# Kernel optimization log

Hardware: AMD Instinct MI355X
Metric: run time of the kernel (lower is better)

The kernel has to match this reference:

```python
import jax, jax.numpy as jnp
import numpy as np

D_MODEL = 1024
N_HEADS = 16
D_K = D_MODEL // N_HEADS
MAX_SEQ = 2048
THETA = 10000.0


def _make_cos_sin():
    # cos_sin[i, k, 0] = cos(i / theta**(2k/d_k)), [.., 1] = sin(...)
    pos = np.arange(MAX_SEQ, dtype=np.float32)[:, None]
    k = np.arange(D_K // 2, dtype=np.float32)[None, :]
    ang = pos / (THETA ** (2.0 * k / D_K))
    return jnp.asarray(np.stack([np.cos(ang), np.sin(ang)], axis=-1), dtype=jnp.float32)


def setup_inputs() -> dict:
    key = jax.random.key(0)
    ks = jax.random.split(key, 5)
    std = 2.0 / (D_MODEL + D_MODEL)
    def w(k):
        return std * jax.random.truncated_normal(k, -3.0, 3.0, (D_MODEL, D_MODEL), dtype=jnp.float32)
    return {
        "x": jax.random.normal(ks[0], (4, 2048, D_MODEL), dtype=jnp.float32),
        "Wq": w(ks[1]),
        "Wk": w(ks[2]),
        "Wv": w(ks[3]),
        "Wo": w(ks[4]),
        "cos_sin": _make_cos_sin(),
        "token_positions": jnp.arange(2048, dtype=jnp.int32),
    }


def _rope(x, cos_sin, pos):
    # x: [B, H, S, d_k]; rotate consecutive pairs
    B, H, S, d = x.shape
    xt = x.reshape(B, H, S, d // 2, 2)
    cos = cos_sin[pos, :, 0]  # [S, d/2]
    sin = cos_sin[pos, :, 1]
    x0, x1 = xt[..., 0], xt[..., 1]
    r0 = cos * x0 - sin * x1
    r1 = sin * x0 + cos * x1
    return jnp.stack([r0, r1], axis=-1).reshape(B, H, S, d)


def reference(x, Wq, Wk, Wv, Wo, cos_sin, token_positions):
    B, S, D = x.shape
    H, d = N_HEADS, D_K
    def proj(W):
        y = jnp.einsum('bsi,oi->bso', x, W)
        return y.reshape(B, S, H, d).transpose(0, 2, 1, 3)  # [B,H,S,d]
    q = _rope(proj(Wq), cos_sin, token_positions)
    k = _rope(proj(Wk), cos_sin, token_positions)
    v = proj(Wv)
    scores = jnp.einsum('bhqd,bhkd->bhqk', q, k) / jnp.sqrt(jnp.float32(d))
    causal = jnp.tril(jnp.ones((S, S), dtype=bool))
    scores = jnp.where(causal, scores, -jnp.inf)
    attn = jax.nn.softmax(scores, axis=-1)
    out = jnp.einsum('bhqk,bhkd->bhqd', attn, v)
    out = out.transpose(0, 2, 1, 3).reshape(B, S, D)
    return jnp.einsum('bsi,oi->bso', out, Wo)
```

## Files before the change

### kernel.cpp

```cpp
#include <hip/hip_runtime.h>

constexpr int B_  = 4;
constexpr int S_  = 2048;
constexpr int D_  = 1024;
constexpr int H_  = 16;
constexpr int DK_ = 64;
constexpr int M_  = B_ * S_;

typedef __attribute__((ext_vector_type(8))) short short8;
typedef __attribute__((ext_vector_type(4))) float f32x4;
typedef __attribute__((ext_vector_type(4))) unsigned short us4;

__device__ __forceinline__ unsigned short f2b(float f) {
  unsigned int u = __float_as_uint(f);
  u += 0x7FFFu + ((u >> 16) & 1u);
  return (unsigned short)(u >> 16);
}
__device__ __forceinline__ float b2f(unsigned short h) {
  return __uint_as_float(((unsigned int)h) << 16);
}
__device__ __forceinline__ unsigned int cvtpk(float lo, float hi) {
  unsigned int w;
  asm("v_cvt_pk_bf16_f32 %0, %1, %2" : "=v"(w) : "v"(lo), "v"(hi));
  return w;
}
__device__ __forceinline__ float exp2v(float x) {
  float r;
  asm("v_exp_f32 %0, %1" : "=v"(r) : "v"(x));
  return r;
}

#define GLOAD16(g, l) __builtin_amdgcn_global_load_lds( \
    (const __attribute__((address_space(1))) unsigned int*)(g), \
    (__attribute__((address_space(3))) unsigned int*)(l), 16, 0, 0)

__global__ __launch_bounds__(256) void conv_kernel(
    const float* __restrict__ x,
    const float* __restrict__ wq, const float* __restrict__ wk, const float* __restrict__ wv,
    unsigned short* __restrict__ xb, unsigned short* __restrict__ wb)
{
  const int NX4 = (M_ * D_) / 4;
  const int NW4 = (3 * D_ * D_) / 4;
  int stride = gridDim.x * blockDim.x;
  for (int i = blockIdx.x * blockDim.x + threadIdx.x; i < NX4 + NW4; i += stride) {
    const float4* src; unsigned short* dst; int o;
    if (i < NX4) { src = (const float4*)x; dst = xb; o = i; }
    else {
      int wi = i - NX4;
      int mat = wi >> 18;
      o = wi & 262143;
      src = (const float4*)(mat == 0 ? wq : (mat == 1 ? wk : wv));
      dst = wb + mat * (D_ * D_);
    }
    float4 v = src[o];
    us4 r; r.x = f2b(v.x); r.y = f2b(v.y); r.z = f2b(v.z); r.w = f2b(v.w);
    *(us4*)(dst + o * 4) = r;
  }
}

__global__ __launch_bounds__(256) void conv_wo_kernel(
    const float* __restrict__ wo, unsigned short* __restrict__ wob)
{
  int i = blockIdx.x * 256 + threadIdx.x;
  float4 v = ((const float4*)wo)[i];
  us4 r; r.x = f2b(v.x); r.y = f2b(v.y); r.z = f2b(v.z); r.w = f2b(v.w);
  *(us4*)(wob + i * 4) = r;
}

__global__ __launch_bounds__(256, 2) void gemm_qkv_kernel(
    const unsigned short* __restrict__ xb,
    const unsigned short* __restrict__ wb,
    const float* __restrict__ cs,
    const int* __restrict__ pos,
    unsigned short* __restrict__ qb,
    unsigned short* __restrict__ kb,
    unsigned short* __restrict__ vtb)
{
  __shared__ unsigned short As[2][128 * 64];
  __shared__ unsigned short Bs[2][128 * 64];
  const int tid  = threadIdx.x;
  const int lane = tid & 63;
  const int wid  = tid >> 6;
  const int wm = wid >> 1, wn = wid & 1;
  const int m0 = blockIdx.x * 128;
  const int n0 = blockIdx.y * 128;
  const int l15 = lane & 15, l4 = lane >> 4;
  const int swz7 = l15 & 7;

  int srow[4], sgcc[4], slds[4];
  #pragma unroll
  for (int j = 0; j < 4; ++j) {
    int c = tid + j * 256;
    srow[j] = c >> 3;
    int cc  = c & 7;
    sgcc[j] = cc ^ (srow[j] & 7);
    slds[j] = (wid * 64 + j * 256) * 8;
  }

  f32x4 acc[4][4] = {};

  #pragma unroll
  for (int j = 0; j < 4; ++j) {
    GLOAD16(xb + (m0 + srow[j]) * D_ + sgcc[j] * 8, &As[0][slds[j]]);
    GLOAD16(wb + (n0 + srow[j]) * D_ + sgcc[j] * 8, &Bs[0][slds[j]]);
  }
  __syncthreads();

  for (int t = 0; t < 16; ++t) {
    const int cur = t & 1, nxt = cur ^ 1;
    if (t < 15) {
      const int kcol = (t + 1) * 64;
      #pragma unroll
      for (int j = 0; j < 4; ++j) {
        GLOAD16(xb + (m0 + srow[j]) * D_ + kcol + sgcc[j] * 8, &As[nxt][slds[j]]);
        GLOAD16(wb + (n0 + srow[j]) * D_ + kcol + sgcc[j] * 8, &Bs[nxt][slds[j]]);
      }
    }
    const unsigned short* Ab = &As[cur][0];
    const unsigned short* Bb = &Bs[cur][0];
    #pragma unroll
    for (int ks = 0; ks < 2; ++ks) {
      const int cc = (ks * 4 + l4) ^ swz7;
      short8 af[4], bfr[4];
      #pragma unroll
      for (int mi = 0; mi < 4; ++mi) af[mi]  = *(const short8*)&Ab[(wm*64 + mi*16 + l15)*64 + cc*8];
      #pragma unroll
      for (int ni = 0; ni < 4; ++ni) bfr[ni] = *(const short8*)&Bb[(wn*64 + ni*16 + l15)*64 + cc*8];
      __builtin_amdgcn_s_setprio(1);
      #pragma unroll
      for (int mi = 0; mi < 4; ++mi)
        #pragma unroll
        for (int ni = 0; ni < 4; ++ni)
          acc[mi][ni] = __builtin_amdgcn_mfma_f32_16x16x32_bf16(af[mi], bfr[ni], acc[mi][ni], 0, 0, 0);
      __builtin_amdgcn_s_setprio(0);
    }
    __syncthreads();
  }

  const int bidx = m0 >> 11;
  const int sbase = (m0 & 2047) + wm * 64;

  if (n0 < 2048) {
    unsigned short* dst = (n0 < 1024) ? qb : kb;
    const int nn0 = n0 & 1023;
    const float2* cs2 = (const float2*)cs;
    const float sg = (l15 & 1) ? 1.0f : -1.0f;
    #pragma unroll
    for (int mi = 0; mi < 4; ++mi)
      #pragma unroll
      for (int j = 0; j < 4; ++j) {
        int s = sbase + mi*16 + l4*4 + j;
        int p = pos[s];
        #pragma unroll
        for (int ni = 0; ni < 4; ++ni) {
          int col = nn0 + wn*64 + ni*16 + l15;
          int h = col >> 6, dd = col & 63;
          float val = acc[mi][ni][j];
          float par = __shfl_xor(val, 1);
          float2 cv = cs2[p*32 + (dd >> 1)];
          float r = fmaf(cv.x, val, sg * cv.y * par);
          dst[((bidx*H_ + h)*S_ + s)*DK_ + dd] = f2b(r);
        }
      }
  } else {
    const int nn0 = n0 & 1023;
    const int hB = (nn0 + wn*64) >> 6;
    #pragma unroll
    for (int mi = 0; mi < 4; ++mi) {
      int s4 = sbase + mi*16 + l4*4;
      #pragma unroll
      for (int ni = 0; ni < 4; ++ni) {
        int dd = ni*16 + l15;
        uint2 w;
        w.x = cvtpk(acc[mi][ni][0], acc[mi][ni][1]);
        w.y = cvtpk(acc[mi][ni][2], acc[mi][ni][3]);
        *(uint2*)(vtb + ((bidx*H_ + hB)*DK_ + dd)*S_ + s4) = w;
      }
    }
  }
}

__global__ __launch_bounds__(256, 4) void attn_kernel(
    const unsigned short* __restrict__ qb,
    const unsigned short* __restrict__ kb,
    const unsigned short* __restrict__ vtb,
    unsigned short* __restrict__ ao)
{
  __shared__ unsigned short Ks[2][64 * 64];
  __shared__ unsigned short Vs[2][64 * 64];
  __shared__ unsigned short Ps[4][16 * 64];
  const int tid = threadIdx.x, lane = tid & 63, wid = tid >> 6;
  const int l15 = lane & 15, l4 = lane >> 4;
  const int swz7 = l15 & 7;

  const int id  = blockIdx.x;
  const int xcd = id & 7, rem = id >> 3;
  const int bh  = xcd * 8 + (rem & 7);
  const int qt  = 15 - (rem >> 3);
  const int q0  = qt * 128;
  const int nkt = 2 * qt + 2;

  const unsigned short* qp = qb  + bh * S_ * DK_;
  const unsigned short* kp = kb  + bh * S_ * DK_;
  const unsigned short* vp = vtb + bh * DK_ * S_;
  const int bidx = bh >> 4, h = bh & 15;

  int srow[2], sgcc[2], slds[2];
  #pragma unroll
  for (int j = 0; j < 2; ++j) {
    int c = tid + j * 256;
    srow[j] = c >> 3;
    int cc  = c & 7;
    sgcc[j] = cc ^ (srow[j] & 7);
    slds[j] = (wid * 64 + j * 256) * 8;
  }

  const float QSC = 0.18033688f;
  short8 qf[2][2];
  #pragma unroll
  for (int y = 0; y < 2; ++y)
    #pragma unroll
    for (int kbk = 0; kbk < 2; ++kbk) {
      short8 raw = *(const short8*)(qp + (q0 + y*64 + wid*16 + l15)*DK_ + kbk*32 + l4*8);
      #pragma unroll
      for (int i = 0; i < 8; ++i) {
        float f = b2f((unsigned short)raw[i]) * QSC;
        raw[i] = (short)f2b(f);
      }
      qf[y][kbk] = raw;
    }

  f32x4 oacc[2][4] = {};
  float mrun[2] = {-1e30f, -1e30f}, lrun[2] = {0.0f, 0.0f};

  #pragma unroll
  for (int j = 0; j < 2; ++j) {
    GLOAD16(kp + srow[j]*DK_ + sgcc[j]*8, &Ks[0][slds[j]]);
    GLOAD16(vp + srow[j]*S_  + sgcc[j]*8, &Vs[0][slds[j]]);
  }
  __syncthreads();

  for (int kt = 0; kt < nkt; ++kt) {
    const int cur = kt & 1, nxt = cur ^ 1;
    if (kt + 1 < nkt) {
      const int kb0 = (kt + 1) * 64;
      #pragma unroll
      for (int j = 0; j < 2; ++j) {
        GLOAD16(kp + (kb0 + srow[j])*DK_ + sgcc[j]*8, &Ks[nxt][slds[j]]);
        GLOAD16(vp + srow[j]*S_ + kb0   + sgcc[j]*8, &Vs[nxt][slds[j]]);
      }
    }

    #pragma unroll
    for (int y = 0; y < 2; ++y) {
      if (kt > 2*qt + y) continue;

      f32x4 sc[4];
      __builtin_amdgcn_s_setprio(1);
      #pragma unroll
      for (int nb = 0; nb < 4; ++nb) {
        const int rb = (nb*16 + l15) * 64;
        short8 k0 = *(const short8*)&Ks[cur][rb + ((l4     ^ swz7) * 8)];
        short8 k1 = *(const short8*)&Ks[cur][rb + (((4+l4) ^ swz7) * 8)];
        f32x4 z = {};
        z = __builtin_amdgcn_mfma_f32_16x16x32_bf16(k0, qf[y][0], z, 0, 0, 0);
        z = __builtin_amdgcn_mfma_f32_16x16x32_bf16(k1, qf[y][1], z, 0, 0, 0);
        sc[nb] = z;
      }
      __builtin_amdgcn_s_setprio(0);

      if (kt == 2*qt + y) {
        const int qg = q0 + y*64 + wid*16 + l15;
        #pragma unroll
        for (int nb = 0; nb < 4; ++nb)
          #pragma unroll
          for (int j = 0; j < 4; ++j) {
            int kg = kt*64 + nb*16 + l4*4 + j;
            if (kg > qg) sc[nb][j] = -1e30f;
          }
      }

      float tm = sc[0][0];
      #pragma unroll
      for (int nb = 0; nb < 4; ++nb)
        #pragma unroll
        for (int j = 0; j < 4; ++j) tm = fmaxf(tm, sc[nb][j]);
      tm = fmaxf(tm, __shfl_xor(tm, 16));
      tm = fmaxf(tm, __shfl_xor(tm, 32));
      if (!__all(tm - mrun[y] <= 8.0f)) {
        float mnew = fmaxf(mrun[y], tm);
        float corr = exp2v(mrun[y] - mnew);
        mrun[y] = mnew;
        lrun[y] *= corr;
        #pragma unroll
        for (int j = 0; j < 4; ++j) {
          float cj = __shfl(corr, l4*4 + j);
          #pragma unroll
          for (int nb = 0; nb < 4; ++nb) oacc[y][nb][j] *= cj;
        }
      }
      float rs = 0.0f;
      #pragma unroll
      for (int nb = 0; nb < 4; ++nb)
        #pragma unroll
        for (int j = 0; j < 4; ++j) {
          float p = exp2v(sc[nb][j] - mrun[y]);
          sc[nb][j] = p;
          rs += p;
        }
      rs += __shfl_xor(rs, 16);
      rs += __shfl_xor(rs, 32);
      lrun[y] += rs;

      #pragma unroll
      for (int nb = 0; nb < 4; ++nb) {
        uint2 w;
        w.x = cvtpk(sc[nb][0], sc[nb][1]);
        w.y = cvtpk(sc[nb][2], sc[nb][3]);
        int ch = nb*2 + (l4 >> 1);
        *(uint2*)&Ps[wid][l15*64 + ((ch ^ swz7) * 8) + (l4 & 1) * 4] = w;
      }
      asm volatile("s_waitcnt lgkmcnt(0)" ::: "memory");
      short8 pa0 = *(const short8*)&Ps[wid][l15*64 + ((l4     ^ swz7) * 8)];
      short8 pa1 = *(const short8*)&Ps[wid][l15*64 + (((4+l4) ^ swz7) * 8)];

      __builtin_amdgcn_s_setprio(1);
      #pragma unroll
      for (int nb = 0; nb < 4; ++nb) {
        const int rb = (nb*16 + l15) * 64;
        short8 v0 = *(const short8*)&Vs[cur][rb + ((l4     ^ swz7) * 8)];
        short8 v1 = *(const short8*)&Vs[cur][rb + (((4+l4) ^ swz7) * 8)];
        oacc[y][nb] = __builtin_amdgcn_mfma_f32_16x16x32_bf16(pa0, v0, oacc[y][nb], 0, 0, 0);
        oacc[y][nb] = __builtin_amdgcn_mfma_f32_16x16x32_bf16(pa1, v1, oacc[y][nb], 0, 0, 0);
      }
      __builtin_amdgcn_s_setprio(0);
    }

    __syncthreads();
  }

  #pragma unroll
  for (int y = 0; y < 2; ++y)
    #pragma unroll
    for (int j = 0; j < 4; ++j) {
      float lj = __shfl(lrun[y], l4*4 + j);
      float inv = 1.0f / lj;
      int row = q0 + y*64 + wid*16 + l4*4 + j;
      #pragma unroll
      for (int nb = 0; nb < 4; ++nb) {
        int dim = nb*16 + l15;
        ao[((bidx*S_ + row)*H_ + h)*DK_ + dim] = f2b(oacc[y][nb][j] * inv);
      }
    }
}

__global__ __launch_bounds__(256, 2) void gemm_out_kernel(
    const unsigned short* __restrict__ ao,
    const unsigned short* __restrict__ wob,
    float* __restrict__ out)
{
  __shared__ unsigned short As[2][128 * 64];
  __shared__ unsigned short Bs[2][128 * 64];
  const int tid = threadIdx.x, lane = tid & 63, wid = tid >> 6;
  const int wm = wid >> 1, wn = wid & 1;
  const int m0 = blockIdx.x * 128, n0 = blockIdx.y * 128;
  const int l15 = lane & 15, l4 = lane >> 4;
  const int swz7 = l15 & 7;

  int srow[4], sgcc[4], slds[4];
  #pragma unroll
  for (int j = 0; j < 4; ++j) {
    int c = tid + j * 256;
    srow[j] = c >> 3;
    int cc  = c & 7;
    sgcc[j] = cc ^ (srow[j] & 7);
    slds[j] = (wid * 64 + j * 256) * 8;
  }

  f32x4 acc[4][4] = {};

  #pragma unroll
  for (int j = 0; j < 4; ++j) {
    GLOAD16(ao  + (m0 + srow[j]) * D_ + sgcc[j] * 8, &As[0][slds[j]]);
    GLOAD16(wob + (n0 + srow[j]) * D_ + sgcc[j] * 8, &Bs[0][slds[j]]);
  }
  __syncthreads();

  for (int t = 0; t < 16; ++t) {
    const int cur = t & 1, nxt = cur ^ 1;
    if (t < 15) {
      const int kcol = (t + 1) * 64;
      #pragma unroll
      for (int j = 0; j < 4; ++j) {
        GLOAD16(ao  + (m0 + srow[j]) * D_ + kcol + sgcc[j] * 8, &As[nxt][slds[j]]);
        GLOAD16(wob + (n0 + srow[j]) * D_ + kcol + sgcc[j] * 8, &Bs[nxt][slds[j]]);
      }
    }
    const unsigned short* Ab = &As[cur][0];
    const unsigned short* Bb = &Bs[cur][0];
    #pragma unroll
    for (int ks = 0; ks < 2; ++ks) {
      const int cc = (ks * 4 + l4) ^ swz7;
      short8 af[4], bfr[4];
      #pragma unroll
      for (int mi = 0; mi < 4; ++mi) af[mi]  = *(const short8*)&Ab[(wm*64 + mi*16 + l15)*64 + cc*8];
      #pragma unroll
      for (int ni = 0; ni < 4; ++ni) bfr[ni] = *(const short8*)&Bb[(wn*64 + ni*16 + l15)*64 + cc*8];
      __builtin_amdgcn_s_setprio(1);
      #pragma unroll
      for (int mi = 0; mi < 4; ++mi)
        #pragma unroll
        for (int ni = 0; ni < 4; ++ni)
          acc[mi][ni] = __builtin_amdgcn_mfma_f32_16x16x32_bf16(af[mi], bfr[ni], acc[mi][ni], 0, 0, 0);
      __builtin_amdgcn_s_setprio(0);
    }
    __syncthreads();
  }

  #pragma unroll
  for (int mi = 0; mi < 4; ++mi)
    #pragma unroll
    for (int ni = 0; ni < 4; ++ni)
      #pragma unroll
      for (int j = 0; j < 4; ++j) {
        int row = m0 + wm*64 + mi*16 + l4*4 + j;
        int col = n0 + wn*64 + ni*16 + l15;
        out[row * D_ + col] = acc[mi][ni][j];
      }
}

extern "C" void kernel_launch(void* const* d_in, const int* in_sizes, int n_in,
                              void* d_out, int out_size, void* d_ws, size_t ws_size,
                              hipStream_t stream)
{
  const float* x  = (const float*)d_in[0];
  const float* wq = (const float*)d_in[1];
  const float* wk = (const float*)d_in[2];
  const float* wv = (const float*)d_in[3];
  const float* wo = (const float*)d_in[4];
  const float* cs = (const float*)d_in[5];
  const int*  pos = (const int*)d_in[6];
  float* out = (float*)d_out;

  unsigned short* xb = (unsigned short*)d_out;
  unsigned short* wb = xb + M_ * D_;

  unsigned short* qb  = (unsigned short*)d_ws;
  unsigned short* kbf = qb  + M_ * D_;
  unsigned short* vtb = kbf + M_ * D_;
  unsigned short* aob = vtb + M_ * D_;
  unsigned short* wob = qb;

  conv_kernel<<<dim3(2048), dim3(256), 0, stream>>>(x, wq, wk, wv, xb, wb);
  gemm_qkv_kernel<<<dim3(64, 24), dim3(256), 0, stream>>>(xb, wb, cs, pos, qb, kbf, vtb);
  attn_kernel<<<dim3(1024), dim3(256), 0, stream>>>(qb, kbf, vtb, aob);
  conv_wo_kernel<<<dim3(1024), dim3(256), 0, stream>>>(wo, wob);
  gemm_out_kernel<<<dim3(64, 8), dim3(256), 0, stream>>>(aob, wob, out);

  (void)in_sizes; (void)n_in; (void)out_size; (void)ws_size;
}
```

Measured before the change: 177.8 us.

## Build P operand in registers by permuting V reads, dropping P LDS round-trip

The softmax probabilities are now packed straight from the score accumulators into the MFMA A operand. The matching V fragments are gathered with 8-byte LDS reads in a permuted k order, so the Ps shared buffer along with its store, wait and reload is removed. Removing Ps cuts shared memory, so launch bounds go from 4 to 5 blocks per CU, and the max and sum reductions are rewritten as trees. The trade-off is twice as many, narrower V reads from LDS, possible bank conflicts, and tighter register limits that could cause spills.

```diff
diff --git a/kernel.cpp b/kernel.cpp
--- a/kernel.cpp
+++ b/kernel.cpp
@@ -10,6 +10,8 @@
 typedef __attribute__((ext_vector_type(8))) short short8;
 typedef __attribute__((ext_vector_type(4))) float f32x4;
 typedef __attribute__((ext_vector_type(4))) unsigned short us4;
+
+union U8 { short8 s8; uint2 p[2]; unsigned int u[4]; };
 
 __device__ __forceinline__ unsigned short f2b(float f) {
   unsigned int u = __float_as_uint(f);
@@ -180,7 +182,7 @@
   }
 }
 
-__global__ __launch_bounds__(256, 4) void attn_kernel(
+__global__ __launch_bounds__(256, 5) void attn_kernel(
     const unsigned short* __restrict__ qb,
     const unsigned short* __restrict__ kb,
     const unsigned short* __restrict__ vtb,
@@ -188,7 +190,6 @@
 {
   __shared__ unsigned short Ks[2][64 * 64];
   __shared__ unsigned short Vs[2][64 * 64];
-  __shared__ unsigned short Ps[4][16 * 64];
   const int tid = threadIdx.x, lane = tid & 63, wid = tid >> 6;
   const int l15 = lane & 15, l4 = lane >> 4;
   const int swz7 = l15 & 7;
@@ -240,6 +241,8 @@
   }
   __syncthreads();
 
+  const int vhalf = (l4 & 1) * 4;
+  const int g0 = l4 >> 1;
   for (int kt = 0; kt < nkt; ++kt) {
     const int cur = kt & 1, nxt = cur ^ 1;
     if (kt + 1 < nkt) {
@@ -280,11 +283,11 @@
           }
       }
 
-      float tm = sc[0][0];
+      float mq[4];
       #pragma unroll
       for (int nb = 0; nb < 4; ++nb)
-        #pragma unroll
-        for (int j = 0; j < 4; ++j) tm = fmaxf(tm, sc[nb][j]);
+        mq[nb] = fmaxf(fmaxf(sc[nb][0], sc[nb][1]), fmaxf(sc[nb][2], sc[nb][3]));
+      float tm = fmaxf(fmaxf(mq[0], mq[1]), fmaxf(mq[2], mq[3]));
       tm = fmaxf(tm, __shfl_xor(tm, 16));
       tm = fmaxf(tm, __shfl_xor(tm, 32));
       if (!__all(tm - mrun[y] <= 8.0f)) {
@@ -299,39 +302,35 @@
           for (int nb = 0; nb < 4; ++nb) oacc[y][nb][j] *= cj;
         }
       }
-      float rs = 0.0f;
-      #pragma unroll
-      for (int nb = 0; nb < 4; ++nb)
-        #pragma unroll
-        for (int j = 0; j < 4; ++j) {
-          float p = exp2v(sc[nb][j] - mrun[y]);
-          sc[nb][j] = p;
-          rs += p;
-        }
+      float sq[4];
+      #pragma unroll
+      for (int nb = 0; nb < 4; ++nb) {
+        #pragma unroll
+        for (int j = 0; j < 4; ++j) sc[nb][j] = exp2v(sc[nb][j] - mrun[y]);
+        sq[nb] = (sc[nb][0] + sc[nb][1]) + (sc[nb][2] + sc[nb][3]);
+      }
+      float rs = (sq[0] + sq[1]) + (sq[2] + sq[3]);
       rs += __shfl_xor(rs, 16);
       rs += __shfl_xor(rs, 32);
       lrun[y] += rs;
 
-      #pragma unroll
-      for (int nb = 0; nb < 4; ++nb) {
-        uint2 w;
-        w.x = cvtpk(sc[nb][0], sc[nb][1]);
-        w.y = cvtpk(sc[nb][2], sc[nb][3]);
-        int ch = nb*2 + (l4 >> 1);
-        *(uint2*)&Ps[wid][l15*64 + ((ch ^ swz7) * 8) + (l4 & 1) * 4] = w;
-      }
-      asm volatile("s_waitcnt lgkmcnt(0)" ::: "memory");
-      short8 pa0 = *(const short8*)&Ps[wid][l15*64 + ((l4     ^ swz7) * 8)];
-      short8 pa1 = *(const short8*)&Ps[wid][l15*64 + (((4+l4) ^ swz7) * 8)];
+      U8 pa0, pa1;
+      pa0.u[0] = cvtpk(sc[0][0], sc[0][1]); pa0.u[1] = cvtpk(sc[0][2], sc[0][3]);
+      pa0.u[2] = cvtpk(sc[1][0], sc[1][1]); pa0.u[3] = cvtpk(sc[1][2], sc[1][3]);
+      pa1.u[0] = cvtpk(sc[2][0], sc[2][1]); pa1.u[1] = cvtpk(sc[2][2], sc[2][3]);
+      pa1.u[2] = cvtpk(sc[3][0], sc[3][1]); pa1.u[3] = cvtpk(sc[3][2], sc[3][3]);
 
       __builtin_amdgcn_s_setprio(1);
       #pragma unroll
       for (int nb = 0; nb < 4; ++nb) {
         const int rb = (nb*16 + l15) * 64;
-        short8 v0 = *(const short8*)&Vs[cur][rb + ((l4     ^ swz7) * 8)];
-        short8 v1 = *(const short8*)&Vs[cur][rb + (((4+l4) ^ swz7) * 8)];
-        oacc[y][nb] = __builtin_amdgcn_mfma_f32_16x16x32_bf16(pa0, v0, oacc[y][nb], 0, 0, 0);
-        oacc[y][nb] = __builtin_amdgcn_mfma_f32_16x16x32_bf16(pa1, v1, oacc[y][nb], 0, 0, 0);
+        U8 v0, v1;
+        v0.p[0] = *(const uint2*)&Vs[cur][rb + (( g0      ^ swz7) * 8) + vhalf];
+        v0.p[1] = *(const uint2*)&Vs[cur][rb + (((2 + g0) ^ swz7) * 8) + vhalf];
+        v1.p[0] = *(const uint2*)&Vs[cur][rb + (((4 + g0) ^ swz7) * 8) + vhalf];
+        v1.p[1] = *(const uint2*)&Vs[cur][rb + (((6 + g0) ^ swz7) * 8) + vhalf];
+        oacc[y][nb] = __builtin_amdgcn_mfma_f32_16x16x32_bf16(pa0.s8, v0.s8, oacc[y][nb], 0, 0, 0);
+        oacc[y][nb] = __builtin_amdgcn_mfma_f32_16x16x32_bf16(pa1.s8, v1.s8, oacc[y][nb], 0, 0, 0);
       }
       __builtin_amdgcn_s_setprio(0);
     }
```

Result: slower. 254.1 us (+42.9%).
